# Performance work log

Measured on AMD Instinct MI355X. Metric: run time of the kernel, lower is better.

Reference implementation:

```python
import jax, jax.numpy as jnp
import numpy as np

B, S, D, H, F = 4, 2048, 512, 8, 2048
HD = D // H
SCALE = HD ** -0.5


def layernorm(x, g, b, eps=1e-5):
    mu = jnp.mean(x, axis=-1, keepdims=True)
    var = jnp.var(x, axis=-1, keepdims=True)
    return (x - mu) * jax.lax.rsqrt(var + eps) * g + b


def setup_inputs() -> dict:
    key = jax.random.key(0)
    ks = jax.random.split(key, 10)
    s = 0.02
    return {
        "x": jax.random.normal(ks[0], (B, S, D), jnp.float32),
        "w_qkv": jax.random.normal(ks[1], (D, 3 * D), jnp.float32) * s,
        "b_qkv": jnp.zeros((3 * D,), jnp.float32),
        "w_o": jax.random.normal(ks[2], (D, D), jnp.float32) * s,
        "b_o": jnp.zeros((D,), jnp.float32),
        "w1": jax.random.normal(ks[3], (D, F), jnp.float32) * s,
        "b1": jnp.zeros((F,), jnp.float32),
        "w2": jax.random.normal(ks[4], (F, D), jnp.float32) * s,
        "b2": jnp.zeros((D,), jnp.float32),
        "g1": jnp.ones((D,), jnp.float32),
        "be1": jnp.zeros((D,), jnp.float32),
        "g2": jnp.ones((D,), jnp.float32),
        "be2": jnp.zeros((D,), jnp.float32),
    }


def reference(x, w_qkv, b_qkv, w_o, b_o, w1, b1, w2, b2, g1, be1, g2, be2):
    res = x
    qkv = x @ w_qkv + b_qkv                       # [B,S,3D]
    q, k, v = jnp.split(qkv, 3, axis=-1)          # each [B,S,D]
    # head partition: [B,S,D] -> [B,H,S,hd]
    def split_heads(t):
        return t.reshape(B, S, H, HD).transpose(0, 2, 1, 3)
    q, k, v = map(split_heads, (q, k, v))
    scores = jnp.einsum('bhqc,bhkc->bhqk', q, k) * SCALE
    weights = jax.nn.softmax(scores, axis=-1)
    out = jnp.einsum('bhqk,bhkc->bhqc', weights, v)
    out = out.transpose(0, 2, 1, 3).reshape(B, S, D)  # merge heads
    out = out @ w_o + b_o
    out = layernorm(out + res, g1, be1)
    res = out
    out = jax.nn.gelu(out @ w1 + b1, approximate=False) @ w2 + b2
    out = layernorm(out + res, g2, be2)
    return out
```

## Files before the change

### kernel.cpp

```cpp
#include <hip/hip_runtime.h>
#include <math.h>

constexpr int B = 4, S = 2048, D = 512, H = 8, HD = 64, F = 2048;
constexpr int M = B * S;
constexpr float C_QK = 0.125f * 1.44269504088896340736f;

typedef __bf16 bf16x8 __attribute__((ext_vector_type(8)));
typedef float  f32x4  __attribute__((ext_vector_type(4)));
typedef float  f32x16 __attribute__((ext_vector_type(16)));

static __device__ __forceinline__ short f2bf(float f) {
  return __builtin_bit_cast(short, (__bf16)f);
}

static __device__ __forceinline__ void gload16(const void* g, void* l) {
  __builtin_amdgcn_global_load_lds(
      (const __attribute__((address_space(1))) unsigned int*)g,
      (__attribute__((address_space(3))) unsigned int*)l, 16, 0, 0);
}

__global__ __launch_bounds__(256)
void prep_all(const float* __restrict__ x, short* __restrict__ xb,
              const float* __restrict__ w_qkv, short* __restrict__ wtq,
              const float* __restrict__ w_o,  short* __restrict__ wto,
              const float* __restrict__ w1,   short* __restrict__ wt1,
              const float* __restrict__ w2,   short* __restrict__ wt2) {
  __shared__ float tl[32][33];
  const int id = blockIdx.x;
  const int t = threadIdx.x;
  if (id < 4096) {
    int i = id * 256 + t;
    float4 v = ((const float4*)x)[i];
    ((short4*)xb)[i] = make_short4(f2bf(v.x), f2bf(v.y), f2bf(v.z), f2bf(v.w));
    return;
  }
  const float* in; short* out; int R, C, bx, by;
  if (id < 4864)      { int k = id - 4096; in = w_qkv; out = wtq; R = 512;  C = 1536; bx = k % 48; by = k / 48; }
  else if (id < 5120) { int k = id - 4864; in = w_o;   out = wto; R = 512;  C = 512;  bx = k % 16; by = k / 16; }
  else if (id < 6144) { int k = id - 5120; in = w1;    out = wt1; R = 512;  C = 2048; bx = k % 64; by = k / 64; }
  else                { int k = id - 6144; in = w2;    out = wt2; R = 2048; C = 512;  bx = k % 16; by = k / 16; }
  const int r0 = by * 32, c0 = bx * 32;
  const int tr = t >> 3, tc4 = (t & 7) * 4;
  float4 v = *(const float4*)&in[(size_t)(r0 + tr) * C + c0 + tc4];
  tl[tr][tc4] = v.x; tl[tr][tc4 + 1] = v.y; tl[tr][tc4 + 2] = v.z; tl[tr][tc4 + 3] = v.w;
  __syncthreads();
  short4 o = make_short4(f2bf(tl[tc4][tr]), f2bf(tl[tc4 + 1][tr]),
                         f2bf(tl[tc4 + 2][tr]), f2bf(tl[tc4 + 3][tr]));
  *(short4*)&out[(size_t)(c0 + tr) * R + r0 + tc4] = o;
}

template<int SPLITK, int GELU, int EPI>
__global__ __launch_bounds__(256)
void gemm_bf16(const short* __restrict__ A, const short* __restrict__ Wt,
               const float* __restrict__ bias,
               float* __restrict__ Cf, short* __restrict__ Cb,
               short* __restrict__ qsw, short* __restrict__ ksw,
               short* __restrict__ vsw, int K, int N, size_t pz) {
  __shared__ short As[128 * 32] __attribute__((aligned(16)));
  __shared__ short Bs[128 * 32] __attribute__((aligned(16)));
  const int t = threadIdx.x;
  const int w = t >> 6, l = t & 63, g = l >> 4, r = l & 15;
  const int wm = w >> 1, wn = w & 1;
  const int m0 = blockIdx.y * 128, n0 = blockIdx.x * 128;
  const int Kc = K / SPLITK;
  const int kstart = blockIdx.z * Kc;

  f32x4 acc[4][4] = {};
  const int NS = Kc >> 5;
  for (int st = 0; st < NS; ++st) {
    const int k0 = kstart + (st << 5);
    __syncthreads();
#pragma unroll
    for (int i = 0; i < 2; ++i) {
      int q = i * 256 + t;
      gload16(A + (size_t)(m0 + (q >> 2)) * K + k0 + (q & 3) * 8, (char*)As + q * 16);
    }
#pragma unroll
    for (int i = 0; i < 2; ++i) {
      int q = i * 256 + t;
      gload16(Wt + (size_t)(n0 + (q >> 2)) * K + k0 + (q & 3) * 8, (char*)Bs + q * 16);
    }
    __syncthreads();
    bf16x8 aF[4], bF[4];
#pragma unroll
    for (int mi = 0; mi < 4; ++mi)
      aF[mi] = *(const bf16x8*)(As + (wm * 64 + mi * 16 + r) * 32 + g * 8);
#pragma unroll
    for (int ni = 0; ni < 4; ++ni)
      bF[ni] = *(const bf16x8*)(Bs + (wn * 64 + ni * 16 + r) * 32 + g * 8);
#pragma unroll
    for (int mi = 0; mi < 4; ++mi)
#pragma unroll
      for (int ni = 0; ni < 4; ++ni)
        acc[mi][ni] = __builtin_amdgcn_mfma_f32_16x16x32_bf16(aF[mi], bF[ni], acc[mi][ni], 0, 0, 0);
  }

  float* Cfz = Cf + (size_t)blockIdx.z * pz;
  const float bscale = (SPLITK > 1 && blockIdx.z != 0) ? 0.0f : 1.0f;
#pragma unroll
  for (int mi = 0; mi < 4; ++mi) {
#pragma unroll
    for (int ni = 0; ni < 4; ++ni) {
      const int n  = n0 + wn * 64 + ni * 16 + r;
      const int mB = m0 + wm * 64 + mi * 16 + g * 4;
      float vals[4];
#pragma unroll
      for (int j = 0; j < 4; ++j) {
        float v = acc[mi][ni][j] + bias[n] * bscale;
        if (GELU) v = 0.5f * v * (1.0f + erff(v * 0.70710678118654752f));
        vals[j] = v;
      }
      if (EPI == 0) {
#pragma unroll
        for (int j = 0; j < 4; ++j) Cfz[(size_t)(mB + j) * N + n] = vals[j];
      } else if (EPI == 1) {
#pragma unroll
        for (int j = 0; j < 4; ++j) Cb[(size_t)(mB + j) * N + n] = f2bf(vals[j]);
      } else {
        const int b = mB >> 11, s = mB & 2047;
        if (n < 512) {
          const int hh = n >> 6, d = n & 63;
          const size_t rb = (size_t)(b * 8 + hh) * 2048;
#pragma unroll
          for (int j = 0; j < 4; ++j)
            qsw[(rb + s + j) * 64 + (d ^ (((s + j) & 7) << 3))] = f2bf(vals[j] * C_QK);
        } else if (n < 1024) {
          const int hh = (n - 512) >> 6, d = (n - 512) & 63;
          const size_t rb = (size_t)(b * 8 + hh) * 2048;
#pragma unroll
          for (int j = 0; j < 4; ++j)
            ksw[(rb + s + j) * 64 + (d ^ (((s + j) & 7) << 3))] = f2bf(vals[j]);
        } else {
          const int hh = (n - 1024) >> 6, d = (n - 1024) & 63;
          short4 pk = make_short4(f2bf(vals[0]), f2bf(vals[1]), f2bf(vals[2]), f2bf(vals[3]));
          *(short4*)&vsw[(size_t)((b * 8 + hh) * 64 + d) * 2048 + (s ^ ((d & 7) << 3))] = pk;
        }
      }
    }
  }
}

__global__ __launch_bounds__(256, 4)
void attn_mfma(const short* __restrict__ qsw, const short* __restrict__ ksw,
               const short* __restrict__ vsw, short* __restrict__ Opart,
               float* __restrict__ Lpart) {
  __shared__ short Ks[64 * 64] __attribute__((aligned(16)));
  __shared__ short Vs[64 * 64] __attribute__((aligned(16)));
  const int t = threadIdx.x;
  const int w = t >> 6, l = t & 63;
  const int c = l & 31, hi = l >> 5;
  const int bh = blockIdx.y;
  const int q0 = blockIdx.x * 128;
  const int kbase = blockIdx.z * 512;
  const short* qb = qsw + ((size_t)bh * 2048 + q0) * 64;
  const short* kb = ksw + (size_t)bh * 2048 * 64;
  const short* vb = vsw + (size_t)bh * 64 * 2048;

  const int qrow = w * 32 + c;
  const int swz = (c & 7) << 3;
  bf16x8 qf[4];
#pragma unroll
  for (int dc = 0; dc < 4; ++dc)
    qf[dc] = *(const bf16x8*)(qb + qrow * 64 + ((dc * 16 + hi * 8) ^ swz));

  f32x16 o0 = {}, o1 = {};
  float m_run = -3e38f, l_run = 0.0f;

  for (int ti = 0; ti < 8; ++ti) {
    const int kt = kbase + ti * 64;
    __syncthreads();
#pragma unroll
    for (int i = 0; i < 2; ++i) {
      int q = i * 256 + t;
      gload16(kb + (size_t)(kt + (q >> 3)) * 64 + (q & 7) * 8, (char*)Ks + q * 16);
    }
#pragma unroll
    for (int i = 0; i < 2; ++i) {
      int q = i * 256 + t;
      gload16(vb + (size_t)(q >> 3) * 2048 + kt + (q & 7) * 8, (char*)Vs + q * 16);
    }
    __syncthreads();

#pragma unroll
    for (int h2 = 0; h2 < 2; ++h2) {
      f32x16 s = {};
      __builtin_amdgcn_s_setprio(1);
#pragma unroll
      for (int dc = 0; dc < 4; ++dc) {
        const int koff = (dc * 16 + hi * 8) ^ swz;
        bf16x8 kf = *(const bf16x8*)(Ks + (h2 * 32 + c) * 64 + koff);
        s = __builtin_amdgcn_mfma_f32_32x32x16_bf16(kf, qf[dc], s, 0, 0, 0);
      }
      __builtin_amdgcn_s_setprio(0);

      float tmax = -3e38f;
#pragma unroll
      for (int j = 0; j < 16; ++j) tmax = fmaxf(tmax, s[j]);
      tmax = fmaxf(tmax, __shfl_xor(tmax, 32, 64));
      if (__any(tmax - m_run > 8.0f)) {
        float mnew = fmaxf(m_run, tmax);
        float rs = __builtin_amdgcn_exp2f(m_run - mnew);
        m_run = mnew;
        l_run *= rs;
#pragma unroll
        for (int j = 0; j < 16; ++j) {
          float rj = __shfl(rs, (j & 3) + 8 * (j >> 2) + 4 * hi, 64);
          o0[j] *= rj; o1[j] *= rj;
        }
      }
      float rsum = 0.0f;
#pragma unroll
      for (int j = 0; j < 16; ++j) {
        s[j] = __builtin_amdgcn_exp2f(s[j] - m_run);
        rsum += s[j];
      }
      rsum += __shfl_xor(rsum, 32, 64);
      l_run += rsum;

      __builtin_amdgcn_s_setprio(1);
#pragma unroll
      for (int kc = 0; kc < 2; ++kc) {
        const int jb = kc * 8;
        int u0, u1, v0, v1;
        asm("v_cvt_pk_bf16_f32 %0, %1, %2" : "=v"(u0) : "v"(s[jb + 0]), "v"(s[jb + 1]));
        asm("v_cvt_pk_bf16_f32 %0, %1, %2" : "=v"(u1) : "v"(s[jb + 2]), "v"(s[jb + 3]));
        asm("v_cvt_pk_bf16_f32 %0, %1, %2" : "=v"(v0) : "v"(s[jb + 4]), "v"(s[jb + 5]));
        asm("v_cvt_pk_bf16_f32 %0, %1, %2" : "=v"(v1) : "v"(s[jb + 6]), "v"(s[jb + 7]));
        asm volatile("v_permlane32_swap_b32 %0, %1" : "+v"(u0), "+v"(v0));
        asm volatile("v_permlane32_swap_b32 %0, %1" : "+v"(u1), "+v"(v1));
        int pw[4] = {u0, u1, v0, v1};
        bf16x8 pa = __builtin_bit_cast(bf16x8, *(int4*)pw);
        const int voff = ((h2 * 32 + kc * 16 + hi * 8)) ^ swz;
        bf16x8 vf0 = *(const bf16x8*)(Vs + c * 64 + voff);
        bf16x8 vf1 = *(const bf16x8*)(Vs + (32 + c) * 64 + voff);
        o0 = __builtin_amdgcn_mfma_f32_32x32x16_bf16(pa, vf0, o0, 0, 0, 0);
        o1 = __builtin_amdgcn_mfma_f32_32x32x16_bf16(pa, vf1, o1, 0, 0, 0);
      }
      __builtin_amdgcn_s_setprio(0);
    }
  }

  const size_t hrow = (size_t)blockIdx.z * (32 * 2048) + (size_t)bh * 2048;
  float inv = 1.0f / l_run;
  if (hi == 0)
    Lpart[hrow + q0 + w * 32 + c] = m_run + __builtin_log2f(l_run);
#pragma unroll
  for (int j = 0; j < 16; ++j) {
    const int q_rel = (j & 3) + 8 * (j >> 2) + 4 * hi;
    float invq = __shfl(inv, q_rel, 64);
    const size_t row = (hrow + q0 + w * 32 + q_rel) * 64;
    Opart[row + c]      = f2bf(o0[j] * invq);
    Opart[row + 32 + c] = f2bf(o1[j] * invq);
  }
}

__global__ __launch_bounds__(256)
void attn_combine(const short* __restrict__ Opart, const float* __restrict__ Lpart,
                  short* __restrict__ a_o) {
  const int idx = blockIdx.x * 256 + threadIdx.x;
  const int row = idx >> 3;
  const int d8 = (idx & 7) * 8;
  float L[4];
#pragma unroll
  for (int z = 0; z < 4; ++z) L[z] = Lpart[z * 65536 + row];
  float mx = fmaxf(fmaxf(L[0], L[1]), fmaxf(L[2], L[3]));
  float wz[4], wsum = 0.0f;
#pragma unroll
  for (int z = 0; z < 4; ++z) { wz[z] = __builtin_amdgcn_exp2f(L[z] - mx); wsum += wz[z]; }
  const float inv = 1.0f / wsum;
  float acc[8] = {};
#pragma unroll
  for (int z = 0; z < 4; ++z) {
    bf16x8 a = *(const bf16x8*)(Opart + ((size_t)z * 65536 + row) * 64 + d8);
#pragma unroll
    for (int i = 0; i < 8; ++i) acc[i] += wz[z] * (float)a[i];
  }
  bf16x8 res;
#pragma unroll
  for (int i = 0; i < 8; ++i) res[i] = (__bf16)(acc[i] * inv);
  const int bh = row >> 11, s = row & 2047;
  const int bb = bh >> 3, hh = bh & 7;
  *(bf16x8*)(a_o + ((size_t)(bb * 2048 + s)) * 512 + hh * 64 + d8) = res;
}

template<int WB, int TWO>
__global__ __launch_bounds__(256)
void add_ln(const float* __restrict__ a, const float* __restrict__ a2,
            const float* __restrict__ res,
            const float* __restrict__ g_, const float* __restrict__ be,
            float* __restrict__ out, short* __restrict__ outb) {
  const int row = blockIdx.x;
  const int t = threadIdx.x;
  const size_t off = (size_t)row * D;
  float x0 = a[off + t] + res[off + t];
  float x1 = a[off + t + 256] + res[off + t + 256];
  if (TWO) { x0 += a2[off + t]; x1 += a2[off + t + 256]; }
  float sum = x0 + x1;
  float sq  = x0 * x0 + x1 * x1;
#pragma unroll
  for (int o2 = 32; o2 > 0; o2 >>= 1) {
    sum += __shfl_down(sum, o2);
    sq  += __shfl_down(sq, o2);
  }
  __shared__ float ssum[4], ssq[4];
  const int wid = t >> 6;
  if ((t & 63) == 0) { ssum[wid] = sum; ssq[wid] = sq; }
  __syncthreads();
  if (t == 0) {
    ssum[0] = ssum[0] + ssum[1] + ssum[2] + ssum[3];
    ssq[0]  = ssq[0] + ssq[1] + ssq[2] + ssq[3];
  }
  __syncthreads();
  float mu   = ssum[0] * (1.0f / D);
  float var  = ssq[0] * (1.0f / D) - mu * mu;
  float rstd = rsqrtf(var + 1e-5f);
  float y0 = (x0 - mu) * rstd * g_[t] + be[t];
  float y1 = (x1 - mu) * rstd * g_[t + 256] + be[t + 256];
  out[off + t] = y0;
  out[off + t + 256] = y1;
  if (WB) {
    outb[off + t] = f2bf(y0);
    outb[off + t + 256] = f2bf(y1);
  }
}

extern "C" void kernel_launch(void* const* d_in, const int* in_sizes, int n_in,
                              void* d_out, int out_size, void* d_ws, size_t ws_size,
                              hipStream_t stream) {
  const float* x     = (const float*)d_in[0];
  const float* w_qkv = (const float*)d_in[1];
  const float* b_qkv = (const float*)d_in[2];
  const float* w_o   = (const float*)d_in[3];
  const float* b_o   = (const float*)d_in[4];
  const float* w1    = (const float*)d_in[5];
  const float* b1    = (const float*)d_in[6];
  const float* w2    = (const float*)d_in[7];
  const float* b2    = (const float*)d_in[8];
  const float* g1    = (const float*)d_in[9];
  const float* be1   = (const float*)d_in[10];
  const float* g2    = (const float*)d_in[11];
  const float* be2   = (const float*)d_in[12];
  float* out = (float*)d_out;
  (void)in_sizes; (void)n_in; (void)out_size; (void)ws_size;

  const size_t MD = (size_t)M * 512;
  short* q_sw = (short*)d_ws;
  short* k_sw = q_sw + MD;
  short* v_sw = k_sw + MD;
  short* a_o  = v_sw + MD;
  short* h    = q_sw;
  short* xb   = a_o + MD;
  short* ln1b = xb;
  short* wtq  = xb + MD;
  short* wto  = wtq + (size_t)1536 * 512;
  short* wt1  = wto + (size_t)512 * 512;
  short* wt2  = wt1 + (size_t)512 * 2048;
  float* buf  = (float*)(wt2 + (size_t)2048 * 512);
  float* ln1  = buf + MD;
  float* buf2 = ln1 + MD;
  float* Lpart = buf2 + MD;
  short* Opart = (short*)buf;

  prep_all<<<7168, 256, 0, stream>>>(x, xb, w_qkv, wtq, w_o, wto, w1, wt1, w2, wt2);

  gemm_bf16<1, 0, 2><<<dim3(12, 64), 256, 0, stream>>>(
      xb, wtq, b_qkv, nullptr, nullptr, q_sw, k_sw, v_sw, 512, 1536, 0);
  attn_mfma<<<dim3(16, 32, 4), 256, 0, stream>>>(q_sw, k_sw, v_sw, Opart, Lpart);
  attn_combine<<<2048, 256, 0, stream>>>(Opart, Lpart, a_o);
  gemm_bf16<2, 0, 0><<<dim3(4, 64, 2), 256, 0, stream>>>(
      a_o, wto, b_o, buf, nullptr, nullptr, nullptr, nullptr, 512, 512, (size_t)2 * MD);
  add_ln<1, 1><<<M, 256, 0, stream>>>(buf, buf2, x, g1, be1, ln1, ln1b);
  gemm_bf16<1, 1, 1><<<dim3(16, 64), 256, 0, stream>>>(
      ln1b, wt1, b1, nullptr, h, nullptr, nullptr, nullptr, 512, 2048, 0);
  gemm_bf16<2, 0, 0><<<dim3(4, 64, 2), 256, 0, stream>>>(
      h, wt2, b2, buf, nullptr, nullptr, nullptr, nullptr, 2048, 512, (size_t)2 * MD);
  add_ln<0, 1><<<M, 256, 0, stream>>>(buf, buf2, ln1, g2, be2, out, nullptr);
}
```

Before: 291.2 us.

## Add 256x256 pipelined GEMM for QKV/FFN and halve attention key splits

Adds a 512-thread GEMM kernel with 256x256 tiles, double-buffered LDS and explicit vmcnt waits, so the next K-slice loads while MFMAs run. It is used for the QKV, FFN1 and split-K=4 FFN2 GEMMs. Attention now uses two key splits instead of four, which shrinks the combine step, and add_ln now sums four split-K partials. Larger tiles cut global traffic per FLOP but launch fewer blocks, which may underfill the CUs, and the bigger LDS footprint limits occupancy.

```diff
diff --git a/kernel.cpp b/kernel.cpp
--- a/kernel.cpp
+++ b/kernel.cpp
@@ -49,13 +49,149 @@
   *(short4*)&out[(size_t)(c0 + tr) * R + r0 + tc4] = o;
 }
 
+template<int GELU, int EPI>
+__global__ __launch_bounds__(512, 2)
+void gemm256(const short* __restrict__ A, const short* __restrict__ Wt,
+             const float* __restrict__ bias,
+             float* __restrict__ Cf, short* __restrict__ Cb,
+             short* __restrict__ qsw, short* __restrict__ ksw,
+             short* __restrict__ vsw, int K, int Kc, int N, size_t pz) {
+  __shared__ short As[2][2][256 * 32] __attribute__((aligned(16)));
+  __shared__ short Bs[2][2][256 * 32] __attribute__((aligned(16)));
+  const int t = threadIdx.x;
+  const int w = t >> 6, l = t & 63, g = l >> 4, r = l & 15;
+  const int wm = w >> 2, wn = w & 3;
+  const int m0 = blockIdx.y * 256, n0 = blockIdx.x * 256;
+  const int kstart = blockIdx.z * Kc;
+  const int NT = Kc >> 6;
+
+  auto stageA = [&](int d, int kh, int tt) {
+    const int k0 = kstart + tt * 64 + kh * 32;
+#pragma unroll
+    for (int i = 0; i < 2; ++i) {
+      int q = i * 512 + t; int row = q >> 2, c16 = q & 3;
+      gload16(A + (size_t)(m0 + row) * K + k0 + c16 * 8, (char*)As[d][kh] + q * 16);
+    }
+  };
+  auto stageB = [&](int d, int kh, int tt) {
+    const int k0 = kstart + tt * 64 + kh * 32;
+#pragma unroll
+    for (int i = 0; i < 2; ++i) {
+      int q = i * 512 + t; int row = q >> 2, c16 = q & 3;
+      gload16(Wt + (size_t)(n0 + row) * K + k0 + c16 * 8, (char*)Bs[d][kh] + q * 16);
+    }
+  };
+
+  f32x4 acc[8][4] = {};
+  bf16x8 aF[4], bF[4];
+
+#define PHASE_MFMA(KH, MG, READB)                                               \
+  {                                                                             \
+    const short* Ah = As[cur][KH];                                              \
+    _Pragma("unroll")                                                           \
+    for (int mi = 0; mi < 4; ++mi)                                              \
+      aF[mi] = *(const bf16x8*)(Ah + (wm * 128 + (MG) * 64 + mi * 16 + r) * 32 + g * 8); \
+    if (READB) {                                                                \
+      const short* Bh = Bs[cur][KH];                                            \
+      _Pragma("unroll")                                                         \
+      for (int ni = 0; ni < 4; ++ni)                                            \
+        bF[ni] = *(const bf16x8*)(Bh + (wn * 64 + ni * 16 + r) * 32 + g * 8);   \
+    }                                                                           \
+    __builtin_amdgcn_s_setprio(1);                                              \
+    _Pragma("unroll")                                                           \
+    for (int mi = 0; mi < 4; ++mi)                                              \
+      _Pragma("unroll")                                                         \
+      for (int ni = 0; ni < 4; ++ni)                                            \
+        acc[(MG) * 4 + mi][ni] = __builtin_amdgcn_mfma_f32_16x16x32_bf16(       \
+            aF[mi], bF[ni], acc[(MG) * 4 + mi][ni], 0, 0, 0);                   \
+    __builtin_amdgcn_s_setprio(0);                                              \
+  }
+
+  stageA(0, 0, 0); stageB(0, 0, 0); stageA(0, 1, 0); stageB(0, 1, 0);
+
+  for (int tt = 0; tt < NT; ++tt) {
+    const int cur = tt & 1, nxt = cur ^ 1;
+    const bool pf = (tt + 1 < NT);
+    if (pf) stageA(nxt, 0, tt + 1);
+    __builtin_amdgcn_sched_barrier(0);
+    if (pf) asm volatile("s_waitcnt vmcnt(6)" ::: "memory");
+    else    asm volatile("s_waitcnt vmcnt(4)" ::: "memory");
+    __builtin_amdgcn_sched_barrier(0);
+    __builtin_amdgcn_s_barrier();
+    __builtin_amdgcn_sched_barrier(0);
+    PHASE_MFMA(0, 0, 1)
+    __builtin_amdgcn_sched_barrier(0);
+    if (pf) stageB(nxt, 0, tt + 1);
+    __builtin_amdgcn_sched_barrier(0);
+    PHASE_MFMA(0, 1, 0)
+    __builtin_amdgcn_sched_barrier(0);
+    if (pf) stageA(nxt, 1, tt + 1);
+    __builtin_amdgcn_sched_barrier(0);
+    if (pf) asm volatile("s_waitcnt vmcnt(6)" ::: "memory");
+    else    asm volatile("s_waitcnt vmcnt(0)" ::: "memory");
+    __builtin_amdgcn_sched_barrier(0);
+    __builtin_amdgcn_s_barrier();
+    __builtin_amdgcn_sched_barrier(0);
+    PHASE_MFMA(1, 0, 1)
+    __builtin_amdgcn_sched_barrier(0);
+    if (pf) stageB(nxt, 1, tt + 1);
+    __builtin_amdgcn_sched_barrier(0);
+    PHASE_MFMA(1, 1, 0)
+    __builtin_amdgcn_s_barrier();
+  }
+#undef PHASE_MFMA
+
+  float* Cfz = Cf + (size_t)blockIdx.z * pz;
+  const float bsc = (blockIdx.z == 0) ? 1.0f : 0.0f;
+#pragma unroll
+  for (int mf = 0; mf < 8; ++mf) {
+#pragma unroll
+    for (int ni = 0; ni < 4; ++ni) {
+      const int n  = n0 + wn * 64 + ni * 16 + r;
+      const int mB = m0 + wm * 128 + mf * 16 + g * 4;
+      float vals[4];
+#pragma unroll
+      for (int j = 0; j < 4; ++j) {
+        float v = acc[mf][ni][j] + bias[n] * bsc;
+        if (GELU) v = 0.5f * v * (1.0f + erff(v * 0.70710678118654752f));
+        vals[j] = v;
+      }
+      if (EPI == 0) {
+#pragma unroll
+        for (int j = 0; j < 4; ++j) Cfz[(size_t)(mB + j) * N + n] = vals[j];
+      } else if (EPI == 1) {
+#pragma unroll
+        for (int j = 0; j < 4; ++j) Cb[(size_t)(mB + j) * N + n] = f2bf(vals[j]);
+      } else {
+        const int b = mB >> 11, s = mB & 2047;
+        if (n < 512) {
+          const int hh = n >> 6, d = n & 63;
+          const size_t rb = (size_t)(b * 8 + hh) * 2048;
+#pragma unroll
+          for (int j = 0; j < 4; ++j)
+            qsw[(rb + s + j) * 64 + (d ^ (((s + j) & 7) << 3))] = f2bf(vals[j] * C_QK);
+        } else if (n < 1024) {
+          const int hh = (n - 512) >> 6, d = (n - 512) & 63;
+          const size_t rb = (size_t)(b * 8 + hh) * 2048;
+#pragma unroll
+          for (int j = 0; j < 4; ++j)
+            ksw[(rb + s + j) * 64 + (d ^ (((s + j) & 7) << 3))] = f2bf(vals[j]);
+        } else {
+          const int hh = (n - 1024) >> 6, d = (n - 1024) & 63;
+          short4 pk = make_short4(f2bf(vals[0]), f2bf(vals[1]), f2bf(vals[2]), f2bf(vals[3]));
+          *(short4*)&vsw[(size_t)((b * 8 + hh) * 64 + d) * 2048 + (s ^ ((d & 7) << 3))] = pk;
+        }
+      }
+    }
+  }
+}
+
 template<int SPLITK, int GELU, int EPI>
 __global__ __launch_bounds__(256)
 void gemm_bf16(const short* __restrict__ A, const short* __restrict__ Wt,
                const float* __restrict__ bias,
                float* __restrict__ Cf, short* __restrict__ Cb,
-               short* __restrict__ qsw, short* __restrict__ ksw,
-               short* __restrict__ vsw, int K, int N, size_t pz) {
+               int K, int N, size_t pz) {
   __shared__ short As[128 * 32] __attribute__((aligned(16)));
   __shared__ short Bs[128 * 32] __attribute__((aligned(16)));
   const int t = threadIdx.x;
@@ -96,45 +232,19 @@
   }
 
   float* Cfz = Cf + (size_t)blockIdx.z * pz;
-  const float bscale = (SPLITK > 1 && blockIdx.z != 0) ? 0.0f : 1.0f;
+  const float bsc = (SPLITK > 1 && blockIdx.z != 0) ? 0.0f : 1.0f;
 #pragma unroll
   for (int mi = 0; mi < 4; ++mi) {
 #pragma unroll
     for (int ni = 0; ni < 4; ++ni) {
       const int n  = n0 + wn * 64 + ni * 16 + r;
       const int mB = m0 + wm * 64 + mi * 16 + g * 4;
-      float vals[4];
 #pragma unroll
       for (int j = 0; j < 4; ++j) {
-        float v = acc[mi][ni][j] + bias[n] * bscale;
+        float v = acc[mi][ni][j] + bias[n] * bsc;
         if (GELU) v = 0.5f * v * (1.0f + erff(v * 0.70710678118654752f));
-        vals[j] = v;
-      }
-      if (EPI == 0) {
-#pragma unroll
-        for (int j = 0; j < 4; ++j) Cfz[(size_t)(mB + j) * N + n] = vals[j];
-      } else if (EPI == 1) {
-#pragma unroll
-        for (int j = 0; j < 4; ++j) Cb[(size_t)(mB + j) * N + n] = f2bf(vals[j]);
-      } else {
-        const int b = mB >> 11, s = mB & 2047;
-        if (n < 512) {
-          const int hh = n >> 6, d = n & 63;
-          const size_t rb = (size_t)(b * 8 + hh) * 2048;
-#pragma unroll
-          for (int j = 0; j < 4; ++j)
-            qsw[(rb + s + j) * 64 + (d ^ (((s + j) & 7) << 3))] = f2bf(vals[j] * C_QK);
-        } else if (n < 1024) {
-          const int hh = (n - 512) >> 6, d = (n - 512) & 63;
-          const size_t rb = (size_t)(b * 8 + hh) * 2048;
-#pragma unroll
-          for (int j = 0; j < 4; ++j)
-            ksw[(rb + s + j) * 64 + (d ^ (((s + j) & 7) << 3))] = f2bf(vals[j]);
-        } else {
-          const int hh = (n - 1024) >> 6, d = (n - 1024) & 63;
-          short4 pk = make_short4(f2bf(vals[0]), f2bf(vals[1]), f2bf(vals[2]), f2bf(vals[3]));
-          *(short4*)&vsw[(size_t)((b * 8 + hh) * 64 + d) * 2048 + (s ^ ((d & 7) << 3))] = pk;
-        }
+        if (EPI == 0) Cfz[(size_t)(mB + j) * N + n] = v;
+        else          Cb[(size_t)(mB + j) * N + n] = f2bf(v);
       }
     }
   }
@@ -151,7 +261,7 @@
   const int c = l & 31, hi = l >> 5;
   const int bh = blockIdx.y;
   const int q0 = blockIdx.x * 128;
-  const int kbase = blockIdx.z * 512;
+  const int kbase = blockIdx.z * 1024;
   const short* qb = qsw + ((size_t)bh * 2048 + q0) * 64;
   const short* kb = ksw + (size_t)bh * 2048 * 64;
   const short* vb = vsw + (size_t)bh * 64 * 2048;
@@ -166,7 +276,7 @@
   f32x16 o0 = {}, o1 = {};
   float m_run = -3e38f, l_run = 0.0f;
 
-  for (int ti = 0; ti < 8; ++ti) {
+  for (int ti = 0; ti < 16; ++ti) {
     const int kt = kbase + ti * 64;
     __syncthreads();
 #pragma unroll
@@ -260,32 +370,25 @@
   const int idx = blockIdx.x * 256 + threadIdx.x;
   const int row = idx >> 3;
   const int d8 = (idx & 7) * 8;
-  float L[4];
-#pragma unroll
-  for (int z = 0; z < 4; ++z) L[z] = Lpart[z * 65536 + row];
-  float mx = fmaxf(fmaxf(L[0], L[1]), fmaxf(L[2], L[3]));
-  float wz[4], wsum = 0.0f;
-#pragma unroll
-  for (int z = 0; z < 4; ++z) { wz[z] = __builtin_amdgcn_exp2f(L[z] - mx); wsum += wz[z]; }
-  const float inv = 1.0f / wsum;
-  float acc[8] = {};
-#pragma unroll
-  for (int z = 0; z < 4; ++z) {
-    bf16x8 a = *(const bf16x8*)(Opart + ((size_t)z * 65536 + row) * 64 + d8);
-#pragma unroll
-    for (int i = 0; i < 8; ++i) acc[i] += wz[z] * (float)a[i];
-  }
+  const float L0 = Lpart[row], L1 = Lpart[65536 + row];
+  const float mx = fmaxf(L0, L1);
+  const float w0 = __builtin_amdgcn_exp2f(L0 - mx), w1 = __builtin_amdgcn_exp2f(L1 - mx);
+  const float inv = 1.0f / (w0 + w1);
+  bf16x8 a = *(const bf16x8*)(Opart + (size_t)row * 64 + d8);
+  bf16x8 b = *(const bf16x8*)(Opart + ((size_t)65536 + row) * 64 + d8);
   bf16x8 res;
 #pragma unroll
-  for (int i = 0; i < 8; ++i) res[i] = (__bf16)(acc[i] * inv);
+  for (int i = 0; i < 8; ++i)
+    res[i] = (__bf16)((w0 * (float)a[i] + w1 * (float)b[i]) * inv);
   const int bh = row >> 11, s = row & 2047;
   const int bb = bh >> 3, hh = bh & 7;
   *(bf16x8*)(a_o + ((size_t)(bb * 2048 + s)) * 512 + hh * 64 + d8) = res;
 }
 
-template<int WB, int TWO>
+template<int WB, int NS>
 __global__ __launch_bounds__(256)
 void add_ln(const float* __restrict__ a, const float* __restrict__ a2,
+            const float* __restrict__ a3, const float* __restrict__ a4,
             const float* __restrict__ res,
             const float* __restrict__ g_, const float* __restrict__ be,
             float* __restrict__ out, short* __restrict__ outb) {
@@ -294,7 +397,9 @@
   const size_t off = (size_t)row * D;
   float x0 = a[off + t] + res[off + t];
   float x1 = a[off + t + 256] + res[off + t + 256];
-  if (TWO) { x0 += a2[off + t]; x1 += a2[off + t + 256]; }
+  if (NS > 1) { x0 += a2[off + t]; x1 += a2[off + t + 256]; }
+  if (NS > 2) { x0 += a3[off + t] + a4[off + t];
+                x1 += a3[off + t + 256] + a4[off + t + 256]; }
   float sum = x0 + x1;
   float sq  = x0 * x0 + x1 * x1;
 #pragma unroll
@@ -356,23 +461,25 @@
   short* wt1  = wto + (size_t)512 * 512;
   short* wt2  = wt1 + (size_t)512 * 2048;
   float* buf  = (float*)(wt2 + (size_t)2048 * 512);
-  float* ln1  = buf + MD;
-  float* buf2 = ln1 + MD;
-  float* Lpart = buf2 + MD;
-  short* Opart = (short*)buf;
+  float* buf2 = buf + MD;
+  float* buf3 = buf2 + MD;
+  float* buf4 = buf3 + MD;
+  float* ln1  = buf4 + MD;
+  short* Opart = (short*)buf3;
+  float* Lpart = buf4;
 
   prep_all<<<7168, 256, 0, stream>>>(x, xb, w_qkv, wtq, w_o, wto, w1, wt1, w2, wt2);
 
-  gemm_bf16<1, 0, 2><<<dim3(12, 64), 256, 0, stream>>>(
-      xb, wtq, b_qkv, nullptr, nullptr, q_sw, k_sw, v_sw, 512, 1536, 0);
-  attn_mfma<<<dim3(16, 32, 4), 256, 0, stream>>>(q_sw, k_sw, v_sw, Opart, Lpart);
+  gemm256<0, 2><<<dim3(6, 32, 1), 512, 0, stream>>>(
+      xb, wtq, b_qkv, nullptr, nullptr, q_sw, k_sw, v_sw, 512, 512, 1536, 0);
+  attn_mfma<<<dim3(16, 32, 2), 256, 0, stream>>>(q_sw, k_sw, v_sw, Opart, Lpart);
   attn_combine<<<2048, 256, 0, stream>>>(Opart, Lpart, a_o);
   gemm_bf16<2, 0, 0><<<dim3(4, 64, 2), 256, 0, stream>>>(
-      a_o, wto, b_o, buf, nullptr, nullptr, nullptr, nullptr, 512, 512, (size_t)2 * MD);
-  add_ln<1, 1><<<M, 256, 0, stream>>>(buf, buf2, x, g1, be1, ln1, ln1b);
-  gemm_bf16<1, 1, 1><<<dim3(16, 64), 256, 0, stream>>>(
-      ln1b, wt1, b1, nullptr, h, nullptr, nullptr, nullptr, 512, 2048, 0);
-  gemm_bf16<2, 0, 0><<<dim3(4, 64, 2), 256, 0, stream>>>(
-      h, wt2, b2, buf, nullptr, nullptr, nullptr, nullptr, 2048, 512, (size_t)2 * MD);
-  add_ln<0, 1><<<M, 256, 0, stream>>>(buf, buf2, ln1, g2, be2, out, nullptr);
-}
+      a_o, wto, b_o, buf, nullptr, 512, 512, MD);
+  add_ln<1, 2><<<M, 256, 0, stream>>>(buf, buf2, nullptr, nullptr, x, g1, be1, ln1, ln1b);
+  gemm256<1, 1><<<dim3(8, 32, 1), 512, 0, stream>>>(
+      ln1b, wt1, b1, nullptr, h, nullptr, nullptr, nullptr, 512, 512, 2048, 0);
+  gemm256<0, 0><<<dim3(2, 32, 4), 512, 0, stream>>>(
+      h, wt2, b2, buf, nullptr, nullptr, nullptr, nullptr, 2048, 512, 512, MD);
+  add_ln<0, 4><<<M, 256, 0, stream>>>(buf, buf2, buf3, buf4, ln1, g2, be2, out, nullptr);
+}
```

Measured after the change: 295.6 us. No clear change (+1.5%).
